# Kernel tuning notes

Hardware: AMD Instinct MI355X
Metric: run time of the kernel (lower is better)

## Reference

```python
import jax, jax.numpy as jnp
import numpy as np

EPS = 1e-5


def spline_conv(x, src, dst, pseudo, W, root, bias, num_nodes, K=5):
    """Degree-1 open B-spline conv (torch_spline_conv semantics), mean aggregation.
    W: [kernel_total, Cin, Cout]. kernel_total==1 means trivial basis (kernel_size=1)."""
    E = src.shape[0]
    Cin = x.shape[1]
    KT = W.shape[0]
    x_j = x[src]                                            # [E, Cin] edge gather
    deg = jax.ops.segment_sum(jnp.ones((E,), x.dtype), dst, num_segments=num_nodes)
    deg = jnp.maximum(deg, 1.0)
    if KT == 1:
        agg = jax.ops.segment_sum(x_j, dst, num_segments=num_nodes)
        out = (agg / deg[:, None]) @ W[0]
    else:
        v = pseudo * (K - 1)                                # open spline: v in [0, K-1]
        f = jnp.clip(jnp.floor(v), 0.0, K - 2)
        frac = v - f                                        # [E, 2]
        fi = f.astype(jnp.int32)
        # bucket basis-weighted source features by (kernel_index, dst) then one dense einsum
        h = jnp.zeros((KT * num_nodes, Cin), x.dtype)
        for s0 in (0, 1):
            for s1 in (0, 1):
                b0 = frac[:, 0] if s0 else 1.0 - frac[:, 0]
                b1 = frac[:, 1] if s1 else 1.0 - frac[:, 1]
                basis = b0 * b1                             # [E]
                wi = (fi[:, 0] + s0) + K * (fi[:, 1] + s1)  # [E] kernel index in [0,25)
                seg = wi * num_nodes + dst
                h = h + jax.ops.segment_sum(basis[:, None] * x_j, seg,
                                            num_segments=KT * num_nodes)
        agg = jnp.einsum('knc,kco->no', h.reshape(KT, num_nodes, Cin), W)
        out = agg / deg[:, None]
    return out + x @ root + bias


def batch_norm(x, gamma, beta):
    m = x.mean(axis=0)
    var = jnp.mean((x - m) ** 2, axis=0)
    return gamma * (x - m) * jax.lax.rsqrt(var + EPS) + beta


def setup_inputs() -> dict:
    key = jax.random.key(0)
    ks = jax.random.split(key, 8)
    N, E, Cin, Cout = 50000, 800000, 32, 64
    x = jax.random.normal(ks[0], (N, Cin), jnp.float32)
    edge_index = jax.random.randint(ks[1], (2, E), 0, N, jnp.int32)
    edge_attr = jax.random.uniform(ks[2], (E, 2), jnp.float32)
    s = 0.1
    return {
        'x': x, 'edge_index': edge_index, 'edge_attr': edge_attr,
        'w1': jax.random.normal(ks[3], (25, Cin, Cout), jnp.float32) * s,
        'r1': jax.random.normal(ks[4], (Cin, Cout), jnp.float32) * s,
        'b1': jnp.zeros((Cout,), jnp.float32),
        'g1': jnp.ones((Cout,), jnp.float32),
        'beta1': jnp.zeros((Cout,), jnp.float32),
        'w2': jax.random.normal(ks[5], (25, Cout, Cout), jnp.float32) * s,
        'r2': jax.random.normal(ks[6], (Cout, Cout), jnp.float32) * s,
        'b2': jnp.zeros((Cout,), jnp.float32),
        'g2': jnp.ones((Cout,), jnp.float32),
        'beta2': jnp.zeros((Cout,), jnp.float32),
        'ws': jax.random.normal(ks[7], (1, Cin, Cout), jnp.float32) * s,
        'rs': jax.random.normal(jax.random.fold_in(key, 99), (Cin, Cout), jnp.float32) * s,
        'bs': jnp.zeros((Cout,), jnp.float32),
        'gs': jnp.ones((Cout,), jnp.float32),
        'betas': jnp.zeros((Cout,), jnp.float32),
    }


def reference(x, edge_index, edge_attr, w1, r1, b1, g1, beta1,
              w2, r2, b2, g2, beta2, ws, rs, bs, gs, betas):
    N = x.shape[0]
    src, dst = edge_index[0], edge_index[1]
    h = jax.nn.elu(batch_norm(spline_conv(x, src, dst, edge_attr, w1, r1, b1, N), g1, beta1))
    left = batch_norm(spline_conv(h, src, dst, edge_attr, w2, r2, b2, N), g2, beta2)
    short = batch_norm(spline_conv(x, src, dst, edge_attr, ws, rs, bs, N), gs, betas)
    return jax.nn.elu(left + short)
```

## Files before the change

kernel.cpp:

```cpp
#include <hip/hip_runtime.h>

#define NN 50000
#define NE 800000

typedef __attribute__((ext_vector_type(8))) short bf16x8;
typedef __attribute__((ext_vector_type(4))) float f32x4;
typedef __attribute__((ext_vector_type(2))) float f32x2;

__device__ __forceinline__ unsigned short f2bf(float f) {
    union { float f; unsigned u; } v; v.f = f;
    unsigned r = v.u + 0x7FFFu + ((v.u >> 16) & 1u);
    return (unsigned short)(r >> 16);
}

__device__ __forceinline__ int4 ld_ep(const int4* ep, unsigned idx) {
    return *(const int4*)((const char*)ep + (size_t)(idx * 16u));
}
__device__ __forceinline__ float ld_x(const float* X, unsigned byteoff) {
    return *(const float*)((const char*)X + (size_t)byteoff);
}

__device__ __forceinline__ int us_idx(int kk, int r, int m) {
    return kk*544 + (r >> 3)*136 + m*8 + (r & 7);
}

template<bool HS>
__device__ __forceinline__ void edge_acc(float* h, float& hs, const int4& p, float x) {
    const f32x2 zero = {0.f, 0.f};
    f32x2 vp = {__int_as_float(p.z), __int_as_float(p.w)};
    f32x2 wxy[5];
#pragma unroll
    for (int r = 0; r < 5; ++r) {
        f32x2 wr = 1.f - __builtin_elementwise_abs(vp - (float)r);
        wxy[r] = __builtin_elementwise_max(wr, zero);
    }
    if (HS) hs += x;
#pragma unroll
    for (int r1 = 0; r1 < 5; ++r1) {
        float ty = x * wxy[r1].y;
#pragma unroll
        for (int r0 = 0; r0 < 5; ++r0)
            h[r1*5 + r0] = fmaf(wxy[r0].x, ty, h[r1*5 + r0]);
    }
}

__global__ __launch_bounds__(256) void k_zero(int* degi, int* cur, float* stats) {
    int i = blockIdx.x*256 + threadIdx.x;
    int stride = gridDim.x*256;
    for (int j = i; j < NN; j += stride) { degi[j] = 0; cur[j] = 0; }
    if (i < 384) stats[i] = 0.f;
}

__global__ __launch_bounds__(256) void k_hist(const int* __restrict__ dst, int* degi) {
    int e = blockIdx.x*256 + threadIdx.x;
    if (e < NE) atomicAdd(&degi[dst[e]], 1);
}

__global__ __launch_bounds__(256) void k_scan_block(const int* __restrict__ degi,
                                                    int* off, int* bsum) {
    __shared__ int sh[256];
    int t = threadIdx.x;
    int base = blockIdx.x * 1024;
    int v[4]; int s = 0;
#pragma unroll
    for (int j = 0; j < 4; j++) {
        int idx = base + t*4 + j;
        v[j] = (idx < NN) ? degi[idx] : 0;
        s += v[j];
    }
    sh[t] = s; __syncthreads();
    for (int ofs = 1; ofs < 256; ofs <<= 1) {
        int x = (t >= ofs) ? sh[t - ofs] : 0;
        __syncthreads();
        sh[t] += x;
        __syncthreads();
    }
    int ex = sh[t] - s;
#pragma unroll
    for (int j = 0; j < 4; j++) {
        int idx = base + t*4 + j;
        if (idx < NN) off[idx] = ex;
        ex += v[j];
    }
    if (t == 255) bsum[blockIdx.x] = sh[255];
}

__global__ __launch_bounds__(256) void k_scan_top(const int* __restrict__ bsum,
                                                  int* bpre, int nb) {
    __shared__ int sh[256];
    int t = threadIdx.x;
    int s = (t < nb) ? bsum[t] : 0;
    sh[t] = s; __syncthreads();
    for (int ofs = 1; ofs < 256; ofs <<= 1) {
        int x = (t >= ofs) ? sh[t - ofs] : 0;
        __syncthreads();
        sh[t] += x;
        __syncthreads();
    }
    if (t < nb) bpre[t] = sh[t] - s;
}

__global__ __launch_bounds__(256) void k_scan_add(int* off, const int* __restrict__ bpre) {
    int i = blockIdx.x*256 + threadIdx.x;
    if (i < NN) off[i] += bpre[i >> 10];
    if (i == 0) off[NN] = NE;
}

__global__ __launch_bounds__(256) void k_scatter(const int* __restrict__ src,
                                                 const int* __restrict__ dst,
                                                 const float* __restrict__ ea,
                                                 const int* __restrict__ off, int* cur,
                                                 int4* __restrict__ ep) {
    int e = blockIdx.x*256 + threadIdx.x;
    if (e >= NE) return;
    int d = dst[e];
    int p = off[d] + atomicAdd(&cur[d], 1);
    float v0 = ea[2*e]     * 4.f;
    float v1 = ea[2*e + 1] * 4.f;
    ep[p] = make_int4(src[e], 0, __float_as_int(v0), __float_as_int(v1));
}

__global__ __launch_bounds__(256) void k_wprep(const float* __restrict__ W,
                                               const float* __restrict__ root,
                                               int KTC, unsigned short* Wb) {
    int tid = blockIdx.x*256 + threadIdx.x;
    int lane = tid & 63, cot = (tid >> 6) & 3, kk = tid >> 8;
    int co = 16*cot + (lane & 15);
    int kbase = kk*32 + ((lane >> 4) * 8);
    union { unsigned short s[8]; uint4 v; } u;
#pragma unroll
    for (int j = 0; j < 8; j++) {
        int k = kbase + j;
        float val = (k < KTC) ? W[(size_t)k*64 + co] : root[(size_t)(k - KTC)*64 + co];
        u.s[j] = f2bf(val);
    }
    *(uint4*)(Wb + (size_t)tid * 8) = u.v;
}

__global__ __launch_bounds__(512, 4) void k_conv1s(
        const float* __restrict__ X,
        const int* __restrict__ off,
        const int4* __restrict__ ep,
        const unsigned short* __restrict__ Wb1,
        const unsigned short* __restrict__ WbS,
        const float* __restrict__ b1,
        const float* __restrict__ bs,
        float* __restrict__ agg1,
        float* __restrict__ aggS) {
    __shared__ __align__(16) unsigned short hb[28*544];
    const int t = threadIdx.x;
    const int g = t >> 5;
    const int ci = t & 31;
    const int n0 = blockIdx.x * 16;
    const int n = n0 + g;

    float h[25], hs = 0.f;
#pragma unroll
    for (int i = 0; i < 25; ++i) h[i] = 0.f;

    const int ebeg = off[n], eend = off[n + 1];
    const int last = eend - 1;
    const float rdeg = 1.f / (float)max(eend - ebeg, 1);

    for (int i = ebeg; i < eend; i += 4) {
        int4 p[4]; float xv[4];
#pragma unroll
        for (int u = 0; u < 4; ++u) p[u] = ld_ep(ep, (unsigned)min(i + u, last));
#pragma unroll
        for (int u = 0; u < 4; ++u) {
            xv[u] = ld_x(X, (unsigned)p[u].x * 128u + (unsigned)ci * 4u);
            if (i + u >= eend) xv[u] = 0.f;
        }
#pragma unroll
        for (int u = 0; u < 4; ++u) edge_acc<true>(h, hs, p[u], xv[u]);
    }

    const int bw = us_idx(0, ci, g);
    const unsigned short xbf = f2bf(X[(size_t)n*32 + ci]);
#pragma unroll
    for (int wi = 0; wi < 25; ++wi) hb[wi*544 + bw] = f2bf(h[wi] * rdeg);
    hb[25*544 + bw] = xbf;
    hb[26*544 + bw] = f2bf(hs * rdeg);
    hb[27*544 + bw] = xbf;
    __syncthreads();

    const int lane = t & 63, w = t >> 6;
    const int m = lane & 15, qq = lane >> 4;
    const int co = (w & 3)*16 + m;
    if (w < 4) {
        f32x4 acc = {0.f, 0.f, 0.f, 0.f};
        for (int kk = 0; kk < 26; ++kk) {
            bf16x8 av = *(const bf16x8*)&hb[kk*544 + qq*136 + m*8];
            bf16x8 bv = *(const bf16x8*)(Wb1 + (size_t)((kk*4 + w)*64 + lane) * 8);
            acc = __builtin_amdgcn_mfma_f32_16x16x32_bf16(av, bv, acc, 0, 0, 0);
        }
        const float bb = b1[co];
#pragma unroll
        for (int r = 0; r < 4; ++r)
            agg1[(size_t)(n0 + qq*4 + r)*64 + co] = acc[r] + bb;
    } else {
        f32x4 accs = {0.f, 0.f, 0.f, 0.f};
#pragma unroll
        for (int s = 0; s < 2; ++s) {
            bf16x8 av = *(const bf16x8*)&hb[(26 + s)*544 + qq*136 + m*8];
            bf16x8 bv = *(const bf16x8*)(WbS + (size_t)((s*4 + (w & 3))*64 + lane) * 8);
            accs = __builtin_amdgcn_mfma_f32_16x16x32_bf16(av, bv, accs, 0, 0, 0);
        }
        const float bb = bs[co];
#pragma unroll
        for (int r = 0; r < 4; ++r)
            aggS[(size_t)(n0 + qq*4 + r)*64 + co] = accs[r] + bb;
    }
}

__global__ __launch_bounds__(512, 4) void k_conv2(
        const float* __restrict__ X,
        const int* __restrict__ off,
        const int4* __restrict__ ep,
        const unsigned short* __restrict__ Wb2,
        const float* __restrict__ b2,
        float* __restrict__ agg) {
    __shared__ __align__(16) unsigned short hb[52*544];
    const int t = threadIdx.x, lane = t & 63, w = t >> 6;
    const int n0 = blockIdx.x * 16;
    const int kh = lane >> 5, r = lane & 31;

#pragma unroll
    for (int nn = 0; nn < 2; ++nn) {
        const int g = 2*w + nn;
        const int n = n0 + g;
        float h[25];
#pragma unroll
        for (int i = 0; i < 25; ++i) h[i] = 0.f;
        float hsd = 0.f;

        const int ebeg = off[n], eend = off[n + 1];
        const int last = eend - 1;
        const float rdeg = 1.f / (float)max(eend - ebeg, 1);

        for (int i = ebeg; i < eend; i += 4) {
            int4 p[4]; float xv[4];
#pragma unroll
            for (int u = 0; u < 4; ++u) p[u] = ld_ep(ep, (unsigned)min(i + u, last));
#pragma unroll
            for (int u = 0; u < 4; ++u) {
                xv[u] = ld_x(X, (unsigned)p[u].x * 256u + (unsigned)lane * 4u);
                if (i + u >= eend) xv[u] = 0.f;
            }
#pragma unroll
            for (int u = 0; u < 4; ++u) edge_acc<false>(h, hsd, p[u], xv[u]);
        }

        const int bw = us_idx(0, r, g);
#pragma unroll
        for (int wi = 0; wi < 25; ++wi)
            hb[(wi*2 + kh)*544 + bw] = f2bf(h[wi] * rdeg);
        hb[(50 + kh)*544 + bw] = f2bf(X[(size_t)n*64 + lane]);
    }
    __syncthreads();

    if (w >= 4) return;

    const int m = lane & 15, qq = lane >> 4;
    f32x4 acc = {0.f, 0.f, 0.f, 0.f};
    for (int kk = 0; kk < 52; ++kk) {
        bf16x8 av = *(const bf16x8*)&hb[kk*544 + qq*136 + m*8];
        bf16x8 bv = *(const bf16x8*)(Wb2 + (size_t)((kk*4 + w)*64 + lane) * 8);
        acc = __builtin_amdgcn_mfma_f32_16x16x32_bf16(av, bv, acc, 0, 0, 0);
    }
    const int co = w*16 + m;
    const float bb = b2[co];
#pragma unroll
    for (int rr = 0; rr < 4; ++rr)
        agg[(size_t)(n0 + qq*4 + rr)*64 + co] = acc[rr] + bb;
}

__global__ __launch_bounds__(256) void k_bnstats(const float* __restrict__ agg, float* stats) {
    __shared__ float sh0[256], sh1[256];
    int t = threadIdx.x;
    float s = 0.f, ss = 0.f;
    int stride = gridDim.x * 256;
    for (int i = blockIdx.x*256 + t; i < NN*64; i += stride) {
        float v = agg[i];
        s += v; ss += v*v;
    }
    sh0[t] = s; sh1[t] = ss;
    __syncthreads();
    if (t < 64) {
        float a = sh0[t] + sh0[t+64] + sh0[t+128] + sh0[t+192];
        float b = sh1[t] + sh1[t+64] + sh1[t+128] + sh1[t+192];
        atomicAdd(&stats[t], a);
        atomicAdd(&stats[64 + t], b);
    }
}

__device__ __forceinline__ float eluf(float u) { return u > 0.f ? u : expm1f(u); }

__global__ __launch_bounds__(256) void k_bn_elu(const float* __restrict__ agg,
                                                const float* __restrict__ stats,
                                                const float* __restrict__ gamma,
                                                const float* __restrict__ beta,
                                                float* __restrict__ out) {
    int i = blockIdx.x*256 + threadIdx.x;
    if (i >= NN*16) return;
    float4 v = ((const float4*)agg)[i];
    float r[4] = {v.x, v.y, v.z, v.w};
    int c0 = (i << 2) & 63;
#pragma unroll
    for (int j = 0; j < 4; j++) {
        int c = c0 + j;
        float mu = stats[c] * (1.f/NN);
        float var = stats[64 + c] * (1.f/NN) - mu*mu;
        float sc = gamma[c] * rsqrtf(fmaxf(var, 0.f) + 1e-5f);
        r[j] = eluf((r[j] - mu)*sc + beta[c]);
    }
    ((float4*)out)[i] = make_float4(r[0], r[1], r[2], r[3]);
}

__global__ __launch_bounds__(256) void k_bn_final(const float* __restrict__ a2,
                                                  const float* __restrict__ st2,
                                                  const float* __restrict__ g2,
                                                  const float* __restrict__ be2,
                                                  const float* __restrict__ as,
                                                  const float* __restrict__ sts,
                                                  const float* __restrict__ gs,
                                                  const float* __restrict__ bes,
                                                  float* __restrict__ out) {
    int i = blockIdx.x*256 + threadIdx.x;
    if (i >= NN*16) return;
    float4 v2 = ((const float4*)a2)[i];
    float4 vs = ((const float4*)as)[i];
    float r2v[4] = {v2.x, v2.y, v2.z, v2.w};
    float rsv[4] = {vs.x, vs.y, vs.z, vs.w};
    float o[4];
    int c0 = (i << 2) & 63;
#pragma unroll
    for (int j = 0; j < 4; j++) {
        int c = c0 + j;
        float mu2 = st2[c] * (1.f/NN);
        float var2 = st2[64 + c] * (1.f/NN) - mu2*mu2;
        float sc2 = g2[c] * rsqrtf(fmaxf(var2, 0.f) + 1e-5f);
        float mus = sts[c] * (1.f/NN);
        float vars = sts[64 + c] * (1.f/NN) - mus*mus;
        float scs = gs[c] * rsqrtf(fmaxf(vars, 0.f) + 1e-5f);
        float u = (r2v[j] - mu2)*sc2 + be2[c] + (rsv[j] - mus)*scs + bes[c];
        o[j] = eluf(u);
    }
    ((float4*)out)[i] = make_float4(o[0], o[1], o[2], o[3]);
}

extern "C" void kernel_launch(void* const* d_in, const int* in_sizes, int n_in,
                              void* d_out, int out_size, void* d_ws, size_t ws_size,
                              hipStream_t stream) {
    const float* x   = (const float*)d_in[0];
    const int*   ei  = (const int*)d_in[1];
    const float* ea  = (const float*)d_in[2];
    const float* w1  = (const float*)d_in[3];
    const float* r1  = (const float*)d_in[4];
    const float* b1  = (const float*)d_in[5];
    const float* g1  = (const float*)d_in[6];
    const float* be1 = (const float*)d_in[7];
    const float* w2  = (const float*)d_in[8];
    const float* r2  = (const float*)d_in[9];
    const float* b2  = (const float*)d_in[10];
    const float* g2  = (const float*)d_in[11];
    const float* be2 = (const float*)d_in[12];
    const float* wsN = (const float*)d_in[13];
    const float* rs  = (const float*)d_in[14];
    const float* bs  = (const float*)d_in[15];
    const float* gs  = (const float*)d_in[16];
    const float* bes = (const float*)d_in[17];
    const int* srcp = ei;
    const int* dstp = ei + NE;

    char* wsb = (char*)d_ws;
    size_t o = 0;
    auto alloc = [&](size_t bytes) -> char* {
        char* p = wsb + o;
        o += (bytes + 255) & ~(size_t)255;
        return p;
    };
    int*    degi    = (int*)   alloc((size_t)NN * 4);
    int*    cur     = (int*)   alloc((size_t)NN * 4);
    int*    off     = (int*)   alloc((size_t)(NN + 1) * 4);
    int*    bsum    = (int*)   alloc(256 * 4);
    int*    bpre    = (int*)   alloc(256 * 4);
    int4*   ep      = (int4*)  alloc((size_t)NE * 16);
    unsigned short* Wb1 = (unsigned short*)alloc(26 * 4096);
    unsigned short* WbS = (unsigned short*)alloc(2 * 4096);
    unsigned short* Wb2 = (unsigned short*)alloc(52 * 4096);
    float*  agg1    = (float*) alloc((size_t)NN * 64 * 4);
    float*  aggS    = (float*) alloc((size_t)NN * 64 * 4);
    float*  h1      = (float*) alloc((size_t)NN * 64 * 4);
    float*  stats   = (float*) alloc(384 * 4);
    (void)ws_size; (void)in_sizes; (void)n_in; (void)out_size;

    float* out = (float*)d_out;

    k_zero<<<196, 256, 0, stream>>>(degi, cur, stats);
    k_hist<<<3125, 256, 0, stream>>>(dstp, degi);
    k_scan_block<<<49, 256, 0, stream>>>(degi, off, bsum);
    k_scan_top<<<1, 256, 0, stream>>>(bsum, bpre, 49);
    k_scan_add<<<196, 256, 0, stream>>>(off, bpre);
    k_scatter<<<3125, 256, 0, stream>>>(srcp, dstp, ea, off, cur, ep);

    k_wprep<<<26, 256, 0, stream>>>(w1, r1, 800, Wb1);
    k_wprep<<<2, 256, 0, stream>>>(wsN, rs, 32, WbS);
    k_wprep<<<52, 256, 0, stream>>>(w2, r2, 1600, Wb2);

    k_conv1s<<<3125, 512, 0, stream>>>(x, off, ep, Wb1, WbS, b1, bs, agg1, aggS);
    k_bnstats<<<256, 256, 0, stream>>>(agg1, stats);
    k_bn_elu<<<3125, 256, 0, stream>>>(agg1, stats, g1, be1, h1);

    k_conv2<<<3125, 512, 0, stream>>>(h1, off, ep, Wb2, b2, agg1);
    k_bnstats<<<256, 256, 0, stream>>>(agg1, stats + 128);
    k_bnstats<<<256, 256, 0, stream>>>(aggS, stats + 256);
    k_bn_final<<<3125, 256, 0, stream>>>(agg1, stats + 128, g2, be2,
                                         aggS, stats + 256, gs, bes, out);
}
```

Measured before the change: 482.4 us.

## Gather node features as packed bf16 pairs and split edges across half-waves

```diff
diff --git a/kernel.cpp b/kernel.cpp
--- a/kernel.cpp
+++ b/kernel.cpp
@@ -16,8 +16,15 @@
 __device__ __forceinline__ int4 ld_ep(const int4* ep, unsigned idx) {
     return *(const int4*)((const char*)ep + (size_t)(idx * 16u));
 }
-__device__ __forceinline__ float ld_x(const float* X, unsigned byteoff) {
-    return *(const float*)((const char*)X + (size_t)byteoff);
+__device__ __forceinline__ unsigned ld_xu(const unsigned* X, unsigned byteoff) {
+    return *(const unsigned*)((const char*)X + (size_t)byteoff);
+}
+
+__device__ __forceinline__ f32x2 unpack2(unsigned u) {
+    union { unsigned u; float f; } a, b;
+    a.u = u << 16;
+    b.u = u & 0xFFFF0000u;
+    return f32x2{a.f, b.f};
 }
 
 __device__ __forceinline__ int us_idx(int kk, int r, int m) {
@@ -25,7 +32,7 @@
 }
 
 template<bool HS>
-__device__ __forceinline__ void edge_acc(float* h, float& hs, const int4& p, float x) {
+__device__ __forceinline__ void edge_acc2(f32x2* h, f32x2& hs, const int4& p, f32x2 x) {
     const f32x2 zero = {0.f, 0.f};
     f32x2 vp = {__int_as_float(p.z), __int_as_float(p.w)};
     f32x2 wxy[5];
@@ -37,11 +44,17 @@
     if (HS) hs += x;
 #pragma unroll
     for (int r1 = 0; r1 < 5; ++r1) {
-        float ty = x * wxy[r1].y;
+        f32x2 ty = x * wxy[r1].y;
 #pragma unroll
         for (int r0 = 0; r0 < 5; ++r0)
-            h[r1*5 + r0] = fmaf(wxy[r0].x, ty, h[r1*5 + r0]);
-    }
+            h[r1*5 + r0] += wxy[r0].x * ty;
+    }
+}
+
+__device__ __forceinline__ float eh_reduce(f32x2 v, int eh, int stride) {
+    float mine  = eh ? v.y : v.x;
+    float other = eh ? v.x : v.y;
+    return mine + __shfl_xor(other, stride);
 }
 
 __global__ __launch_bounds__(256) void k_zero(int* degi, int* cur, float* stats) {
@@ -120,6 +133,17 @@
     ep[p] = make_int4(src[e], 0, __float_as_int(v0), __float_as_int(v1));
 }
 
+__global__ __launch_bounds__(256) void k_xbf(const float* __restrict__ x,
+                                             unsigned short* __restrict__ xb) {
+    int i = blockIdx.x*256 + threadIdx.x;
+    if (i >= NN*8) return;
+    float4 v = ((const float4*)x)[i];
+    uint2 pk;
+    pk.x = (unsigned)f2bf(v.x) | ((unsigned)f2bf(v.y) << 16);
+    pk.y = (unsigned)f2bf(v.z) | ((unsigned)f2bf(v.w) << 16);
+    ((uint2*)xb)[i] = pk;
+}
+
 __global__ __launch_bounds__(256) void k_wprep(const float* __restrict__ W,
                                                const float* __restrict__ root,
                                                int KTC, unsigned short* Wb) {
@@ -138,7 +162,7 @@
 }
 
 __global__ __launch_bounds__(512, 4) void k_conv1s(
-        const float* __restrict__ X,
+        const unsigned* __restrict__ Xbf,
         const int* __restrict__ off,
         const int4* __restrict__ ep,
         const unsigned short* __restrict__ Wb1,
@@ -150,38 +174,45 @@
     __shared__ __align__(16) unsigned short hb[28*544];
     const int t = threadIdx.x;
     const int g = t >> 5;
-    const int ci = t & 31;
+    const int q = t & 31;
+    const int chp = q & 15;
+    const int eh = q >> 4;
     const int n0 = blockIdx.x * 16;
     const int n = n0 + g;
 
-    float h[25], hs = 0.f;
-#pragma unroll
-    for (int i = 0; i < 25; ++i) h[i] = 0.f;
+    f32x2 h[25], hs = {0.f, 0.f};
+#pragma unroll
+    for (int i = 0; i < 25; ++i) h[i] = f32x2{0.f, 0.f};
 
     const int ebeg = off[n], eend = off[n + 1];
     const int last = eend - 1;
     const float rdeg = 1.f / (float)max(eend - ebeg, 1);
 
     for (int i = ebeg; i < eend; i += 4) {
-        int4 p[4]; float xv[4];
-#pragma unroll
-        for (int u = 0; u < 4; ++u) p[u] = ld_ep(ep, (unsigned)min(i + u, last));
-#pragma unroll
-        for (int u = 0; u < 4; ++u) {
-            xv[u] = ld_x(X, (unsigned)p[u].x * 128u + (unsigned)ci * 4u);
-            if (i + u >= eend) xv[u] = 0.f;
-        }
-#pragma unroll
-        for (int u = 0; u < 4; ++u) edge_acc<true>(h, hs, p[u], xv[u]);
-    }
-
-    const int bw = us_idx(0, ci, g);
-    const unsigned short xbf = f2bf(X[(size_t)n*32 + ci]);
-#pragma unroll
-    for (int wi = 0; wi < 25; ++wi) hb[wi*544 + bw] = f2bf(h[wi] * rdeg);
-    hb[25*544 + bw] = xbf;
-    hb[26*544 + bw] = f2bf(hs * rdeg);
-    hb[27*544 + bw] = xbf;
+        const int e0 = i + eh, e1 = i + 2 + eh;
+        int4 p0 = ld_ep(ep, (unsigned)min(e0, last));
+        int4 p1 = ld_ep(ep, (unsigned)min(e1, last));
+        unsigned u0 = ld_xu(Xbf, (unsigned)p0.x * 64u + (unsigned)chp * 4u);
+        unsigned u1 = ld_xu(Xbf, (unsigned)p1.x * 64u + (unsigned)chp * 4u);
+        if (e0 > last) u0 = 0u;
+        if (e1 > last) u1 = 0u;
+        edge_acc2<true>(h, hs, p0, unpack2(u0));
+        edge_acc2<true>(h, hs, p1, unpack2(u1));
+    }
+
+    const int c = 2*chp + eh;
+    const int bw = us_idx(0, c, g);
+#pragma unroll
+    for (int wi = 0; wi < 25; ++wi)
+        hb[wi*544 + bw] = f2bf(eh_reduce(h[wi], eh, 16) * rdeg);
+    hb[26*544 + bw] = f2bf(eh_reduce(hs, eh, 16) * rdeg);
+    {
+        unsigned ux = Xbf[(unsigned)n * 16u + (unsigned)chp];
+        unsigned short xb = eh ? (unsigned short)(ux >> 16)
+                               : (unsigned short)(ux & 0xFFFFu);
+        hb[25*544 + bw] = xb;
+        hb[27*544 + bw] = xb;
+    }
     __syncthreads();
 
     const int lane = t & 63, w = t >> 6;
@@ -214,7 +245,7 @@
 }
 
 __global__ __launch_bounds__(512, 4) void k_conv2(
-        const float* __restrict__ X,
+        const unsigned* __restrict__ Xbf,
         const int* __restrict__ off,
         const int4* __restrict__ ep,
         const unsigned short* __restrict__ Wb2,
@@ -223,39 +254,43 @@
     __shared__ __align__(16) unsigned short hb[52*544];
     const int t = threadIdx.x, lane = t & 63, w = t >> 6;
     const int n0 = blockIdx.x * 16;
-    const int kh = lane >> 5, r = lane & 31;
+    const int chp = lane & 31, eh = lane >> 5;
+    const int c = 2*chp + eh;
+    const int kh = c >> 5, r = c & 31;
 
 #pragma unroll
     for (int nn = 0; nn < 2; ++nn) {
         const int g = 2*w + nn;
         const int n = n0 + g;
-        float h[25];
-#pragma unroll
-        for (int i = 0; i < 25; ++i) h[i] = 0.f;
-        float hsd = 0.f;
+        f32x2 h[25]; f32x2 hsd = {0.f, 0.f};
+#pragma unroll
+        for (int i = 0; i < 25; ++i) h[i] = f32x2{0.f, 0.f};
 
         const int ebeg = off[n], eend = off[n + 1];
         const int last = eend - 1;
         const float rdeg = 1.f / (float)max(eend - ebeg, 1);
 
         for (int i = ebeg; i < eend; i += 4) {
-            int4 p[4]; float xv[4];
-#pragma unroll
-            for (int u = 0; u < 4; ++u) p[u] = ld_ep(ep, (unsigned)min(i + u, last));
-#pragma unroll
-            for (int u = 0; u < 4; ++u) {
-                xv[u] = ld_x(X, (unsigned)p[u].x * 256u + (unsigned)lane * 4u);
-                if (i + u >= eend) xv[u] = 0.f;
-            }
-#pragma unroll
-            for (int u = 0; u < 4; ++u) edge_acc<false>(h, hsd, p[u], xv[u]);
+            const int e0 = i + eh, e1 = i + 2 + eh;
+            int4 p0 = ld_ep(ep, (unsigned)min(e0, last));
+            int4 p1 = ld_ep(ep, (unsigned)min(e1, last));
+            unsigned u0 = ld_xu(Xbf, (unsigned)p0.x * 128u + (unsigned)chp * 4u);
+            unsigned u1 = ld_xu(Xbf, (unsigned)p1.x * 128u + (unsigned)chp * 4u);
+            if (e0 > last) u0 = 0u;
+            if (e1 > last) u1 = 0u;
+            edge_acc2<false>(h, hsd, p0, unpack2(u0));
+            edge_acc2<false>(h, hsd, p1, unpack2(u1));
         }
 
         const int bw = us_idx(0, r, g);
 #pragma unroll
         for (int wi = 0; wi < 25; ++wi)
-            hb[(wi*2 + kh)*544 + bw] = f2bf(h[wi] * rdeg);
-        hb[(50 + kh)*544 + bw] = f2bf(X[(size_t)n*64 + lane]);
+            hb[(wi*2 + kh)*544 + bw] = f2bf(eh_reduce(h[wi], eh, 32) * rdeg);
+        {
+            unsigned ux = Xbf[(unsigned)n * 32u + (unsigned)chp];
+            hb[(50 + kh)*544 + bw] =
+                (unsigned short)(eh ? (ux >> 16) : (ux & 0xFFFFu));
+        }
     }
     __syncthreads();
 
@@ -300,7 +335,7 @@
                                                 const float* __restrict__ stats,
                                                 const float* __restrict__ gamma,
                                                 const float* __restrict__ beta,
-                                                float* __restrict__ out) {
+                                                unsigned short* __restrict__ outb) {
     int i = blockIdx.x*256 + threadIdx.x;
     if (i >= NN*16) return;
     float4 v = ((const float4*)agg)[i];
@@ -314,7 +349,10 @@
         float sc = gamma[c] * rsqrtf(fmaxf(var, 0.f) + 1e-5f);
         r[j] = eluf((r[j] - mu)*sc + beta[c]);
     }
-    ((float4*)out)[i] = make_float4(r[0], r[1], r[2], r[3]);
+    uint2 pk;
+    pk.x = (unsigned)f2bf(r[0]) | ((unsigned)f2bf(r[1]) << 16);
+    pk.y = (unsigned)f2bf(r[2]) | ((unsigned)f2bf(r[3]) << 16);
+    ((uint2*)outb)[i] = pk;
 }
 
 __global__ __launch_bounds__(256) void k_bn_final(const float* __restrict__ a2,
@@ -391,7 +429,8 @@
     unsigned short* Wb2 = (unsigned short*)alloc(52 * 4096);
     float*  agg1    = (float*) alloc((size_t)NN * 64 * 4);
     float*  aggS    = (float*) alloc((size_t)NN * 64 * 4);
-    float*  h1      = (float*) alloc((size_t)NN * 64 * 4);
+    unsigned short* h1bf = (unsigned short*)alloc((size_t)NN * 64 * 2);
+    unsigned short* xbf  = (unsigned short*)alloc((size_t)NN * 32 * 2);
     float*  stats   = (float*) alloc(384 * 4);
     (void)ws_size; (void)in_sizes; (void)n_in; (void)out_size;
 
@@ -404,15 +443,17 @@
     k_scan_add<<<196, 256, 0, stream>>>(off, bpre);
     k_scatter<<<3125, 256, 0, stream>>>(srcp, dstp, ea, off, cur, ep);
 
+    k_xbf<<<1563, 256, 0, stream>>>(x, xbf);
     k_wprep<<<26, 256, 0, stream>>>(w1, r1, 800, Wb1);
     k_wprep<<<2, 256, 0, stream>>>(wsN, rs, 32, WbS);
     k_wprep<<<52, 256, 0, stream>>>(w2, r2, 1600, Wb2);
 
-    k_conv1s<<<3125, 512, 0, stream>>>(x, off, ep, Wb1, WbS, b1, bs, agg1, aggS);
+    k_conv1s<<<3125, 512, 0, stream>>>((const unsigned*)xbf, off, ep, Wb1, WbS,
+                                       b1, bs, agg1, aggS);
     k_bnstats<<<256, 256, 0, stream>>>(agg1, stats);
-    k_bn_elu<<<3125, 256, 0, stream>>>(agg1, stats, g1, be1, h1);
-
-    k_conv2<<<3125, 512, 0, stream>>>(h1, off, ep, Wb2, b2, agg1);
+    k_bn_elu<<<3125, 256, 0, stream>>>(agg1, stats, g1, be1, h1bf);
+
+    k_conv2<<<3125, 512, 0, stream>>>((const unsigned*)h1bf, off, ep, Wb2, b2, agg1);
     k_bnstats<<<256, 256, 0, stream>>>(agg1, stats + 128);
     k_bnstats<<<256, 256, 0, stream>>>(aggS, stats + 256);
     k_bn_final<<<3125, 256, 0, stream>>>(agg1, stats + 128, g2, be2,
```

After: 451.8 us. 6.3% less time.
